# Optimization experiments

Measured on AMD Instinct MI355X. Metric: run time of the kernel, lower is better.

The kernel has to match this reference:

```python
import jax, jax.numpy as jnp
import numpy as np

NEG = -9e10


def _gat_layer(h_in, adj_mask, W, a, alpha, concat):
    # h_in: [N, Fin], W: [Fin, Fout], a: [2*Fout, 1]
    h = h_in @ W                                  # [N, Fout]
    Fout = W.shape[1]
    a1 = a[:Fout, 0]                              # [Fout]
    a2 = a[Fout:, 0]                              # [Fout]
    # e[i,j] = leakyrelu(h_i . a1 + h_j . a2)  (decomposed repeat+cat score)
    s1 = h @ a1                                   # [N]
    s2 = h @ a2                                   # [N]
    e = jax.nn.leaky_relu(s1[:, None] + s2[None, :], negative_slope=alpha)  # [N, N]
    e = jnp.where(adj_mask, e, NEG)
    att = jax.nn.softmax(e, axis=1)               # [N, N]
    h_prime = att @ h                             # [N, Fout]
    return jax.nn.elu(h_prime) if concat else h_prime


def setup_inputs() -> dict:
    key = jax.random.key(0)
    ks = jax.random.split(key, 6)
    N, nfeat, nhid, nheads, nout = 4096, 512, 64, 8, 56
    x = jax.random.normal(ks[0], (N, nfeat), dtype=jnp.float32)
    adj = jax.random.randint(ks[1], (N, N), 0, 2, dtype=jnp.int32)
    Ws = jax.random.normal(ks[2], (nheads, nfeat, nhid), dtype=jnp.float32) * 0.05
    As = jax.random.normal(ks[3], (nheads, 2 * nhid, 1), dtype=jnp.float32) * 0.05
    W_out = jax.random.normal(ks[4], (nhid, nout), dtype=jnp.float32) * 0.05
    a_out = jax.random.normal(ks[5], (2 * nout, 1), dtype=jnp.float32) * 0.05
    return {"x": x, "adj": adj, "Ws": Ws, "As": As, "W_out": W_out, "a_out": a_out}


def reference(x, adj, Ws, As, W_out, a_out):
    alpha = 0.2
    nheads = Ws.shape[0]
    adj_mask = adj > 0
    # dropout is identity in eval mode
    heads = jax.vmap(lambda W, a: _gat_layer(x, adj_mask, W, a, alpha, True))(Ws, As)
    z = jnp.sum(heads, axis=0) / nheads           # [N, nhid] (heads averaged, per source)
    out = _gat_layer(z, adj_mask, W_out, a_out, alpha, False)
    out = jax.nn.elu(out)                         # [N, 56]
    return jax.nn.softmax(out, axis=1)
```

## Files before the change

kernel.cpp:

```cpp
#include <hip/hip_runtime.h>
#include <hip/hip_bf16.h>
#include <math.h>


#define GN 4096
#define GNH 8
#define LOG2E 1.4426950408889634f

typedef __bf16 bf16x8 __attribute__((ext_vector_type(8)));
typedef float f32x4 __attribute__((ext_vector_type(4)));

#if defined(__has_builtin)
#if __has_builtin(__builtin_amdgcn_exp2f)
#define FAST_EXP2(x) __builtin_amdgcn_exp2f(x)
#endif
#if __has_builtin(__builtin_amdgcn_perm)
#define FAST_PERM(a, b, s) __builtin_amdgcn_perm((a), (b), (s))
#endif
#endif
#ifndef FAST_EXP2
#define FAST_EXP2(x) __expf((x)*0.6931471805599453f)
#endif
#ifndef FAST_PERM
__device__ inline unsigned FAST_PERM(unsigned a, unsigned b, unsigned) {
    return (a & 0xFFFF0000u) | (b >> 16);
}
#endif

__device__ inline unsigned hi_pack2(float w0, float w1) {
    unsigned u0 = __float_as_uint(w0) + 0x8000u;
    unsigned u1 = __float_as_uint(w1) + 0x8000u;
    return FAST_PERM(u1, u0, 0x07060302u);
}

__global__ __launch_bounds__(256) void prep(const int* __restrict__ adj,
                                            const float* __restrict__ x,
                                            const float* __restrict__ Ws,
                                            unsigned long long* __restrict__ adjb,
                                            unsigned short* __restrict__ xh,
                                            unsigned short* __restrict__ wth) {
    const int b = blockIdx.x;
    const int tid = threadIdx.x;
    if (b < 16384) {
        const int wv = tid >> 6, lane = tid & 63;
        const size_t ebase = ((size_t)b * 4 + wv) * 256;
        unsigned long long m[4];
        #pragma unroll
        for (int e = 0; e < 4; ++e)
            m[e] = __ballot(adj[ebase + e * 64 + lane] > 0);
        if (lane == 0) {
            #pragma unroll
            for (int e = 0; e < 4; ++e) adjb[(ebase >> 6) + e] = m[e];
        }
    } else if (b < 17408) {
        int gid = (b - 16384) * 256 + tid;
        int i = gid >> 6, c64 = gid & 63;
        const float* xp = x + (size_t)i * 512 + c64 * 8;
        float4 a = *(const float4*)xp;
        float4 v = *(const float4*)(xp + 4);
        unsigned hp[4];
        hp[0] = hi_pack2(a.x, a.y);
        hp[1] = hi_pack2(a.z, a.w);
        hp[2] = hi_pack2(v.x, v.y);
        hp[3] = hi_pack2(v.z, v.w);
        int il = i & 63, kt = c64 >> 3, c = c64 & 7;
        size_t base = ((size_t)(i >> 6) * 8 + kt) * 4096 + il * 64 + ((c ^ (il & 7)) * 8);
        *(uint4*)&xh[base] = *(uint4*)hp;
    } else {
        __shared__ float t[64][65];
        int b2 = b - 17408;
        int head = b2 >> 3, k0 = (b2 & 7) * 64;
        #pragma unroll
        for (int it = 0; it < 4; ++it) {
            int e = (tid + it * 256) * 4;
            int kl = e >> 6, f4 = e & 63;
            float4 v = *(const float4*)&Ws[((size_t)head * 512 + k0 + kl) * 64 + f4];
            t[f4 + 0][kl] = v.x; t[f4 + 1][kl] = v.y;
            t[f4 + 2][kl] = v.z; t[f4 + 3][kl] = v.w;
        }
        __syncthreads();
        int f = tid >> 2;
        #pragma unroll
        for (int p = 0; p < 2; ++p) {
            int c = (tid & 3) * 2 + p;
            unsigned hp[4];
            #pragma unroll
            for (int pp = 0; pp < 4; ++pp)
                hp[pp] = hi_pack2(t[f][c * 8 + 2 * pp], t[f][c * 8 + 2 * pp + 1]);
            size_t base = (size_t)b2 * 4096 + f * 64 + ((c ^ (f & 7)) * 8);
            *(uint4*)&wth[base] = *(uint4*)hp;
        }
    }
}

__global__ __launch_bounds__(256) void gemm_fused(const unsigned short* __restrict__ xh,
                                                  const unsigned short* __restrict__ wth,
                                                  const float* __restrict__ As,
                                                  unsigned short* __restrict__ imgh,
                                                  float* __restrict__ rL,
                                                  float2* __restrict__ ebL) {
    __shared__ __align__(16) unsigned short lds[2][2][4096];
    const int tid = threadIdx.x;
    const int head = blockIdx.x;
    const int itile = blockIdx.y;
    const int i0 = itile * 64;
    const unsigned short* srcs[2] = {xh + (size_t)itile * 8 * 4096,
                                     wth + (size_t)head * 8 * 4096};
    const int lane = tid & 63, wv_ = tid >> 6;
    const int mi = (wv_ & 1) * 32, fi = (wv_ >> 1) * 32;
    const int row = lane & 15, quad = lane >> 4;
    f32x4 acc[2][2] = {};

    #define GSTAGE(buf, kt)                                                                \
        do {                                                                               \
            _Pragma("unroll")                                                              \
            for (int q_ = 0; q_ < 2; ++q_) {                                               \
                const unsigned short* s_ = srcs[q_] + (size_t)(kt) * 4096;                 \
                _Pragma("unroll")                                                          \
                for (int c_ = 0; c_ < 2; ++c_)                                             \
                    __builtin_amdgcn_global_load_lds(                                      \
                        (const __attribute__((address_space(1))) unsigned int*)(s_ + c_ * 2048 + tid * 8), \
                        (__attribute__((address_space(3))) unsigned int*)&lds[buf][q_][c_ * 2048 + tid * 8], \
                        16, 0, 0);                                                         \
            }                                                                              \
        } while (0)

    GSTAGE(0, 0);
    for (int kt = 0; kt < 8; ++kt) {
        __syncthreads();
        const int cur = kt & 1;
        if (kt + 1 < 8) GSTAGE(cur ^ 1, kt + 1);
        #pragma unroll
        for (int ks = 0; ks < 2; ++ks) {
            bf16x8 ah[2], bh[2];
            #pragma unroll
            for (int t = 0; t < 2; ++t) {
                const int m_ = mi + t * 16 + row;
                const int offa = m_ * 64 + (((ks * 4 + quad) ^ (m_ & 7)) * 8);
                ah[t] = *(const bf16x8*)&lds[cur][0][offa];
                const int f_ = fi + t * 16 + row;
                const int offb = f_ * 64 + (((ks * 4 + quad) ^ (f_ & 7)) * 8);
                bh[t] = *(const bf16x8*)&lds[cur][1][offb];
            }
            #pragma unroll
            for (int mt = 0; mt < 2; ++mt)
                #pragma unroll
                for (int nt = 0; nt < 2; ++nt)
                    acc[mt][nt] = __builtin_amdgcn_mfma_f32_16x16x32_bf16(ah[mt], bh[nt], acc[mt][nt], 0, 0, 0);
        }
    }
    #undef GSTAGE
    __syncthreads();
    float* ht = (float*)&lds[0][0][0];
    #pragma unroll
    for (int mt = 0; mt < 2; ++mt)
        #pragma unroll
        for (int nt = 0; nt < 2; ++nt)
            #pragma unroll
            for (int r = 0; r < 4; ++r)
                ht[(mi + mt * 16 + quad * 4 + r) * 68 + fi + nt * 16 + row] = acc[mt][nt][r];
    __syncthreads();
    {
        const int rrow = tid >> 2, seg = (tid & 3) * 16;
        const float* ah = As + head * 128;
        float p1 = 0.f, p2 = 0.f;
        #pragma unroll
        for (int c = 0; c < 16; ++c) {
            float v = ht[rrow * 68 + seg + c];
            p1 += v * ah[seg + c];
            p2 += v * ah[64 + seg + c];
        }
        p1 += __shfl_xor(p1, 1); p1 += __shfl_xor(p1, 2);
        p2 += __shfl_xor(p2, 1); p2 += __shfl_xor(p2, 2);
        if ((tid & 3) == 0) {
            const int gi = i0 + rrow;
            rL[head * GN + gi] = FAST_EXP2(0.8f * p1 * LOG2E);
            float2 e;
            e.x = FAST_EXP2(p2 * LOG2E);
            e.y = FAST_EXP2(0.2f * p2 * LOG2E);
            ebL[head * GN + gi] = e;
        }
    }
    {
        const int f = tid >> 2;
        size_t base = ((size_t)head * 64 + itile) * 4096 + (size_t)f * 64;
        #pragma unroll
        for (int p = 0; p < 2; ++p) {
            int c = (tid & 3) * 2 + p;
            unsigned hp[4];
            #pragma unroll
            for (int pp = 0; pp < 4; ++pp)
                hp[pp] = hi_pack2(ht[(c * 8 + 2 * pp) * 68 + f], ht[(c * 8 + 2 * pp + 1) * 68 + f]);
            int off = (c ^ (f & 7)) * 8;
            *(uint4*)&imgh[base + off] = *(uint4*)hp;
        }
    }
}

template <int NCHUNK>
__global__ __launch_bounds__(256, 4) void attn10(const unsigned short* __restrict__ imgh,
                                                 const float* __restrict__ rg,
                                                 const float2* __restrict__ ebg,
                                                 const unsigned long long* __restrict__ adjb,
                                                 float* __restrict__ pO,
                                                 float* __restrict__ pd) {
    __shared__ __align__(16) unsigned short hb[2][8192];
    const int tid = threadIdx.x;
    const int lane = tid & 63, wv = tid >> 6;
    const int row = lane & 15, quad = lane >> 4;
    const int head = blockIdx.y / NCHUNK;
    const int chunk = blockIdx.y % NCHUNK;
    const int i0 = blockIdx.x * 64;
    const int jb = chunk * (GN / NCHUNK);
    const int njt = (GN / NCHUNK) / 64;
    const int njp = njt >> 1;
    const int jt0 = jb >> 6;
    const unsigned short* ih = imgh + (size_t)head * (64 * GN);
    const float2* ebh = ebg + (size_t)head * GN;
    const int gr = i0 + wv * 16 + row;
    const float rv = rg[head * GN + gr];
    const unsigned long long* adjr = adjb + (size_t)gr * 64 + jt0;

    f32x4 acc[4] = {};
    f32x4 accd = {};
    union { unsigned u[4]; bf16x8 v; } ones;
    #pragma unroll
    for (int q = 0; q < 4; ++q) ones.u[q] = 0x3F803F80u;

    #define STAGE2(buf, T)                                                                 \
        do {                                                                               \
            const unsigned short* gh_ = ih + (size_t)(T) * 4096;                           \
            _Pragma("unroll")                                                              \
            for (int c_ = 0; c_ < 4; ++c_)                                                 \
                __builtin_amdgcn_global_load_lds(                                          \
                    (const __attribute__((address_space(1))) unsigned int*)(gh_ + c_ * 2048 + tid * 8), \
                    (__attribute__((address_space(3))) unsigned int*)&hb[buf][c_ * 2048 + tid * 8],     \
                    16, 0, 0);                                                             \
        } while (0)

    #define CTILE(cur, half, WD, F00, F01, F02, F03, F10, F11, F12, F13)                   \
        do {                                                                               \
            _Pragma("unroll")                                                              \
            for (int ks = 0; ks < 2; ++ks) {                                               \
                const int kb = ks * 32 + quad * 8;                                         \
                const unsigned bits = (unsigned)((WD) >> kb) & 0xFFu;                      \
                const float4 e4[4] = {ks ? F10 : F00, ks ? F11 : F01,                      \
                                      ks ? F12 : F02, ks ? F13 : F03};                     \
                union { unsigned u[4]; bf16x8 v; } wfr;                                    \
                _Pragma("unroll")                                                          \
                for (int p = 0; p < 4; ++p) {                                              \
                    const float4 e = e4[p];                          \
                    const float m0 = (float)((bits >> (2 * p)) & 1u);                      \
                    const float m1 = (float)((bits >> (2 * p + 1)) & 1u);                  \
                    const float w0 = fmaxf(rv * e.x, e.y) * m0;                            \
                    const float w1 = fmaxf(rv * e.z, e.w) * m1;                            \
                    wfr.u[p] = hi_pack2(w0, w1);                                           \
                }                                                                          \
                accd = __builtin_amdgcn_mfma_f32_16x16x32_bf16(wfr.v, ones.v, accd, 0, 0, 0); \
                _Pragma("unroll")                                                          \
                for (int nt = 0; nt < 4; ++nt) {                                           \
                    const int f = nt * 16 + row;                                           \
                    const int off = (half) * 4096 + f * 64 + (((ks * 4 + quad) ^ (f & 7)) * 8); \
                    bf16x8 bh = *(const bf16x8*)&hb[cur][off];                             \
                    acc[nt] = __builtin_amdgcn_mfma_f32_16x16x32_bf16(wfr.v, bh, acc[nt], 0, 0, 0); \
                }                                                                          \
            }                                                                              \
        } while (0)

    STAGE2(0, jt0);
    const float2* ebp = ebh + jb + quad * 8;
    unsigned long long wdn = adjr[0];
    float4 n00 = *(const float4*)(ebp + 0);
    float4 n01 = *(const float4*)(ebp + 2);
    float4 n02 = *(const float4*)(ebp + 4);
    float4 n03 = *(const float4*)(ebp + 6);
    float4 n10 = *(const float4*)(ebp + 32);
    float4 n11 = *(const float4*)(ebp + 34);
    float4 n12 = *(const float4*)(ebp + 36);
    float4 n13 = *(const float4*)(ebp + 38);

    for (int ph = 0; ph < njp; ++ph) {
        __syncthreads();
        const int cur = ph & 1;
        if (ph + 1 < njp) STAGE2(cur ^ 1, jt0 + 2 * (ph + 1));
        {
            const unsigned long long wd = wdn;
            const float4 f00 = n00, f01 = n01, f02 = n02, f03 = n03;
            const float4 f10 = n10, f11 = n11, f12 = n12, f13 = n13;
            {
                const int tn = 2 * ph + 1;
                wdn = adjr[tn];
                const float2* ebn = ebp + tn * 64;
                n00 = *(const float4*)(ebn + 0);
                n01 = *(const float4*)(ebn + 2);
                n02 = *(const float4*)(ebn + 4);
                n03 = *(const float4*)(ebn + 6);
                n10 = *(const float4*)(ebn + 32);
                n11 = *(const float4*)(ebn + 34);
                n12 = *(const float4*)(ebn + 36);
                n13 = *(const float4*)(ebn + 38);
            }
            CTILE(cur, 0, wd, f00, f01, f02, f03, f10, f11, f12, f13);
        }
        {
            const unsigned long long wd = wdn;
            const float4 f00 = n00, f01 = n01, f02 = n02, f03 = n03;
            const float4 f10 = n10, f11 = n11, f12 = n12, f13 = n13;
            if (ph + 1 < njp) {
                const int tn = 2 * ph + 2;
                wdn = adjr[tn];
                const float2* ebn = ebp + tn * 64;
                n00 = *(const float4*)(ebn + 0);
                n01 = *(const float4*)(ebn + 2);
                n02 = *(const float4*)(ebn + 4);
                n03 = *(const float4*)(ebn + 6);
                n10 = *(const float4*)(ebn + 32);
                n11 = *(const float4*)(ebn + 34);
                n12 = *(const float4*)(ebn + 36);
                n13 = *(const float4*)(ebn + 38);
            }
            CTILE(cur, 1, wd, f00, f01, f02, f03, f10, f11, f12, f13);
        }
    }
    #undef STAGE2
    #undef CTILE
    float* o = pO + (size_t)blockIdx.y * (GN * 64);
    #pragma unroll
    for (int r = 0; r < 4; ++r) {
        const int grow = i0 + wv * 16 + quad * 4 + r;
        #pragma unroll
        for (int nt = 0; nt < 4; ++nt)
            o[(size_t)grow * 64 + nt * 16 + row] = acc[nt][r];
    }
    if (row == 0) {
        #pragma unroll
        for (int r = 0; r < 4; ++r)
            pd[blockIdx.y * GN + i0 + wv * 16 + quad * 4 + r] = accd[r];
    }
}

__global__ __launch_bounds__(256) void mid(const float* __restrict__ pO,
                                           const float* __restrict__ pd,
                                           const float* __restrict__ Wo,
                                           const float* __restrict__ ao,
                                           unsigned short* __restrict__ img2h,
                                           float* __restrict__ rbL,
                                           float2* __restrict__ eb2L) {
    __shared__ __align__(16) float zt[16][68];
    __shared__ float Wl[64 * 57];
    __shared__ float invd[8][16];
    const int tid = threadIdx.x;
    const int i0 = blockIdx.x * 16;
    for (int idx = tid; idx < 64 * 56; idx += 256) {
        int k = idx / 56, c = idx - k * 56;
        Wl[k * 57 + c] = Wo[idx];
    }
    if (tid < 128) {
        int hd = tid >> 4, r = tid & 15;
        invd[hd][r] = 1.f / (pd[(2 * hd) * GN + i0 + r] + pd[(2 * hd + 1) * GN + i0 + r]);
    }
    __syncthreads();
    #pragma unroll
    for (int it = 0; it < 4; ++it) {
        int e = it * 256 + tid;
        int r = e >> 6, f = e & 63;
        size_t base = (size_t)(i0 + r) * 64 + f;
        float s = 0.f;
        #pragma unroll
        for (int hd = 0; hd < GNH; ++hd) {
            float o = pO[(size_t)(2 * hd) * (GN * 64) + base] +
                      pO[(size_t)(2 * hd + 1) * (GN * 64) + base];
            float v = o * invd[hd][r];
            s += v > 0.f ? v : FAST_EXP2(v * LOG2E) - 1.f;
        }
        zt[r][f] = s * 0.125f;
    }
    __syncthreads();
    const int rrow = tid >> 4, cseg = (tid & 15) * 4;
    float hreg[4] = {0.f, 0.f, 0.f, 0.f};
    for (int k0 = 0; k0 < 64; k0 += 4) {
        float4 zv = *(const float4*)&zt[rrow][k0];
        #pragma unroll
        for (int c = 0; c < 4; ++c) {
            int col = cseg + c;
            if (col < 56)
                hreg[c] += zv.x * Wl[k0 * 57 + col] + zv.y * Wl[(k0 + 1) * 57 + col] +
                           zv.z * Wl[(k0 + 2) * 57 + col] + zv.w * Wl[(k0 + 3) * 57 + col];
        }
    }
    {
        float p1 = 0.f, p2 = 0.f;
        #pragma unroll
        for (int c = 0; c < 4; ++c) {
            int col = cseg + c;
            if (col < 56) {
                p1 += hreg[c] * ao[col];
                p2 += hreg[c] * ao[56 + col];
            }
        }
        p1 += __shfl_xor(p1, 1); p1 += __shfl_xor(p1, 2);
        p1 += __shfl_xor(p1, 4); p1 += __shfl_xor(p1, 8);
        p2 += __shfl_xor(p2, 1); p2 += __shfl_xor(p2, 2);
        p2 += __shfl_xor(p2, 4); p2 += __shfl_xor(p2, 8);
        if ((tid & 15) == 0) {
            rbL[i0 + rrow] = FAST_EXP2(0.8f * p1 * LOG2E);
            float2 e;
            e.x = FAST_EXP2(p2 * LOG2E);
            e.y = FAST_EXP2(0.2f * p2 * LOG2E);
            eb2L[i0 + rrow] = e;
        }
    }
    __syncthreads();
    #pragma unroll
    for (int c = 0; c < 4; ++c) zt[rrow][cseg + c] = (cseg + c < 56) ? hreg[c] : 0.f;
    __syncthreads();
    if (tid < 128) {
        const int jt = i0 >> 6;
        const int cbase = (i0 & 63) >> 3;
        const int f = tid >> 1, c = cbase + (tid & 1);
        const int lr = (tid & 1) * 8;
        unsigned hp[4];
        #pragma unroll
        for (int pp = 0; pp < 4; ++pp)
            hp[pp] = hi_pack2(zt[lr + 2 * pp][f], zt[lr + 2 * pp + 1][f]);
        size_t base = (size_t)jt * 4096 + f * 64 + ((c ^ (f & 7)) * 8);
        *(uint4*)&img2h[base] = *(uint4*)hp;
    }
}

__global__ __launch_bounds__(256) void fink2(const float* __restrict__ pO,
                                             const float* __restrict__ pd,
                                             float* __restrict__ out) {
    const int lane = threadIdx.x & 63;
    const int w = threadIdx.x >> 6;
    const int i = blockIdx.x * 4 + w;
    float o = 0.f, d = 0.f;
    #pragma unroll
    for (int c = 0; c < 16; ++c) d += pd[c * GN + i];
    if (lane < 56) {
        #pragma unroll
        for (int c = 0; c < 16; ++c) o += pO[(size_t)c * (GN * 64) + (size_t)i * 64 + lane];
    }
    float v = -1e30f;
    if (lane < 56) {
        float t = o / d;
        v = t > 0.f ? t : expm1f(t);
    }
    float m = v;
    #pragma unroll
    for (int off = 32; off; off >>= 1) m = fmaxf(m, __shfl_down(m, off));
    m = __shfl(m, 0);
    float p = (lane < 56) ? __expf(v - m) : 0.f;
    float s = p;
    #pragma unroll
    for (int off = 32; off; off >>= 1) s += __shfl_down(s, off);
    s = __shfl(s, 0);
    if (lane < 56) out[(size_t)i * 56 + lane] = p / s;
}

extern "C" void kernel_launch(void* const* d_in, const int* in_sizes, int n_in,
                              void* d_out, int out_size, void* d_ws, size_t ws_size,
                              hipStream_t stream) {
    const float* x    = (const float*)d_in[0];
    const int*   adj  = (const int*)d_in[1];
    const float* Ws   = (const float*)d_in[2];
    const float* As   = (const float*)d_in[3];
    const float* Wo   = (const float*)d_in[4];
    const float* ao   = (const float*)d_in[5];
    float* out = (float*)d_out;

    char* ws = (char*)d_ws;
    unsigned long long* adjb = (unsigned long long*)(ws + 0);
    unsigned short* img1h = (unsigned short*)(ws + 2097152);
    float* pO    = (float*)(ws + 6291456);
    unsigned short* x_hi = (unsigned short*)(ws + 6291456);
    float* pd    = (float*)(ws + 23068672);
    float* rL    = (float*)(ws + 23330816);
    float2* ebL  = (float2*)(ws + 23461888);
    float* rbL   = (float*)(ws + 23724032);
    float2* eb2L = (float2*)(ws + 23740416);
    unsigned short* img2h = (unsigned short*)(ws + 23773184);
    unsigned short* WT_hi = (unsigned short*)(ws + 24297472);

    prep<<<17472, 256, 0, stream>>>(adj, x, Ws, adjb, x_hi, WT_hi);
    gemm_fused<<<dim3(8, 64), 256, 0, stream>>>(x_hi, WT_hi, As, img1h, rL, ebL);
    attn10<2><<<dim3(64, 16), 256, 0, stream>>>(img1h, rL, ebL, adjb, pO, pd);
    mid<<<256, 256, 0, stream>>>(pO, pd, Wo, ao, img2h, rbL, eb2L);
    attn10<16><<<dim3(64, 16), 256, 0, stream>>>(img2h, rbL, eb2L, adjb, pO, pd);
    fink2<<<1024, 256, 0, stream>>>(pO, pd, out);
}
```

Baseline: 205.6 us.

## Switch operands to fp16 and compute attention weights with packed half math

Replaces bf16 truncation packing with fp16 packed conversion (cvt_pkrtz) and uses fp16 MFMA everywhere. The per-column exp factors are stored as packed fp16 pairs, which halves their load traffic in the attention kernel. The weight computation now uses packed half max/multiply with bit masks instead of float ops, converts and float-to-int mask multiplies. The risk is fp16 range overflow for exp values and accuracy differences.

Result: faster. 185.2 us (-9.9%).

```diff
diff --git a/kernel.cpp b/kernel.cpp
--- a/kernel.cpp
+++ b/kernel.cpp
@@ -7,7 +7,9 @@
 #define GNH 8
 #define LOG2E 1.4426950408889634f
 
-typedef __bf16 bf16x8 __attribute__((ext_vector_type(8)));
+typedef _Float16 f16x8 __attribute__((ext_vector_type(8)));
+typedef _Float16 f16x2 __attribute__((ext_vector_type(2)));
+typedef __fp16 fp16x2_raw __attribute__((ext_vector_type(2)));
 typedef float f32x4 __attribute__((ext_vector_type(4)));
 
 #if defined(__has_builtin)
@@ -15,22 +17,29 @@
 #define FAST_EXP2(x) __builtin_amdgcn_exp2f(x)
 #endif
 #if __has_builtin(__builtin_amdgcn_perm)
-#define FAST_PERM(a, b, s) __builtin_amdgcn_perm((a), (b), (s))
+#define MASK_PERM(h, l) __builtin_amdgcn_perm((h), (l), 0x05040100u)
+#endif
+#if __has_builtin(__builtin_amdgcn_cvt_pkrtz)
+#define HAVE_PKRTZ 1
 #endif
 #endif
 #ifndef FAST_EXP2
 #define FAST_EXP2(x) __expf((x)*0.6931471805599453f)
 #endif
-#ifndef FAST_PERM
-__device__ inline unsigned FAST_PERM(unsigned a, unsigned b, unsigned) {
-    return (a & 0xFFFF0000u) | (b >> 16);
-}
-#endif
-
-__device__ inline unsigned hi_pack2(float w0, float w1) {
-    unsigned u0 = __float_as_uint(w0) + 0x8000u;
-    unsigned u1 = __float_as_uint(w1) + 0x8000u;
-    return FAST_PERM(u1, u0, 0x07060302u);
+#ifndef MASK_PERM
+#define MASK_PERM(h, l) (((h) & 0xFFFF0000u) | ((l) & 0xFFFFu))
+#endif
+
+__device__ inline unsigned pk_f16(float a, float b) {
+#ifdef HAVE_PKRTZ
+    union { fp16x2_raw h; unsigned u; } r;
+    r.h = __builtin_amdgcn_cvt_pkrtz(a, b);
+    return r.u;
+#else
+    union { _Float16 h; unsigned short s; } x, y;
+    x.h = (_Float16)a; y.h = (_Float16)b;
+    return (unsigned)x.s | ((unsigned)y.s << 16);
+#endif
 }
 
 __global__ __launch_bounds__(256) void prep(const int* __restrict__ adj,
@@ -59,10 +68,10 @@
         float4 a = *(const float4*)xp;
         float4 v = *(const float4*)(xp + 4);
         unsigned hp[4];
-        hp[0] = hi_pack2(a.x, a.y);
-        hp[1] = hi_pack2(a.z, a.w);
-        hp[2] = hi_pack2(v.x, v.y);
-        hp[3] = hi_pack2(v.z, v.w);
+        hp[0] = pk_f16(a.x, a.y);
+        hp[1] = pk_f16(a.z, a.w);
+        hp[2] = pk_f16(v.x, v.y);
+        hp[3] = pk_f16(v.z, v.w);
         int il = i & 63, kt = c64 >> 3, c = c64 & 7;
         size_t base = ((size_t)(i >> 6) * 8 + kt) * 4096 + il * 64 + ((c ^ (il & 7)) * 8);
         *(uint4*)&xh[base] = *(uint4*)hp;
@@ -86,7 +95,7 @@
             unsigned hp[4];
             #pragma unroll
             for (int pp = 0; pp < 4; ++pp)
-                hp[pp] = hi_pack2(t[f][c * 8 + 2 * pp], t[f][c * 8 + 2 * pp + 1]);
+                hp[pp] = pk_f16(t[f][c * 8 + 2 * pp], t[f][c * 8 + 2 * pp + 1]);
             size_t base = (size_t)b2 * 4096 + f * 64 + ((c ^ (f & 7)) * 8);
             *(uint4*)&wth[base] = *(uint4*)hp;
         }
@@ -98,7 +107,7 @@
                                                   const float* __restrict__ As,
                                                   unsigned short* __restrict__ imgh,
                                                   float* __restrict__ rL,
-                                                  float2* __restrict__ ebL) {
+                                                  uint2* __restrict__ ebL) {
     __shared__ __align__(16) unsigned short lds[2][2][4096];
     const int tid = threadIdx.x;
     const int head = blockIdx.x;
@@ -132,21 +141,21 @@
         if (kt + 1 < 8) GSTAGE(cur ^ 1, kt + 1);
         #pragma unroll
         for (int ks = 0; ks < 2; ++ks) {
-            bf16x8 ah[2], bh[2];
+            f16x8 ah[2], bh[2];
             #pragma unroll
             for (int t = 0; t < 2; ++t) {
                 const int m_ = mi + t * 16 + row;
                 const int offa = m_ * 64 + (((ks * 4 + quad) ^ (m_ & 7)) * 8);
-                ah[t] = *(const bf16x8*)&lds[cur][0][offa];
+                ah[t] = *(const f16x8*)&lds[cur][0][offa];
                 const int f_ = fi + t * 16 + row;
                 const int offb = f_ * 64 + (((ks * 4 + quad) ^ (f_ & 7)) * 8);
-                bh[t] = *(const bf16x8*)&lds[cur][1][offb];
+                bh[t] = *(const f16x8*)&lds[cur][1][offb];
             }
             #pragma unroll
             for (int mt = 0; mt < 2; ++mt)
                 #pragma unroll
                 for (int nt = 0; nt < 2; ++nt)
-                    acc[mt][nt] = __builtin_amdgcn_mfma_f32_16x16x32_bf16(ah[mt], bh[nt], acc[mt][nt], 0, 0, 0);
+                    acc[mt][nt] = __builtin_amdgcn_mfma_f32_16x16x32_f16(ah[mt], bh[nt], acc[mt][nt], 0, 0, 0);
         }
     }
     #undef GSTAGE
@@ -172,13 +181,18 @@
         }
         p1 += __shfl_xor(p1, 1); p1 += __shfl_xor(p1, 2);
         p2 += __shfl_xor(p2, 1); p2 += __shfl_xor(p2, 2);
-        if ((tid & 3) == 0) {
-            const int gi = i0 + rrow;
-            rL[head * GN + gi] = FAST_EXP2(0.8f * p1 * LOG2E);
-            float2 e;
-            e.x = FAST_EXP2(p2 * LOG2E);
-            e.y = FAST_EXP2(0.2f * p2 * LOG2E);
-            ebL[head * GN + gi] = e;
+        const float r_ = FAST_EXP2(0.8f * p1 * LOG2E);
+        const float B_ = FAST_EXP2(p2 * LOG2E);
+        const float b_ = FAST_EXP2(0.2f * p2 * LOG2E);
+        const float Bo = __shfl_xor(B_, 4);
+        const float bo = __shfl_xor(b_, 4);
+        const int gi = i0 + rrow;
+        if ((tid & 3) == 0) rL[head * GN + gi] = r_;
+        if ((tid & 7) == 0) {
+            uint2 e;
+            e.x = pk_f16(B_, Bo);
+            e.y = pk_f16(b_, bo);
+            ebL[head * (GN / 2) + (gi >> 1)] = e;
         }
     }
     {
@@ -190,7 +204,7 @@
             unsigned hp[4];
             #pragma unroll
             for (int pp = 0; pp < 4; ++pp)
-                hp[pp] = hi_pack2(ht[(c * 8 + 2 * pp) * 68 + f], ht[(c * 8 + 2 * pp + 1) * 68 + f]);
+                hp[pp] = pk_f16(ht[(c * 8 + 2 * pp) * 68 + f], ht[(c * 8 + 2 * pp + 1) * 68 + f]);
             int off = (c ^ (f & 7)) * 8;
             *(uint4*)&imgh[base + off] = *(uint4*)hp;
         }
@@ -198,9 +212,9 @@
 }
 
 template <int NCHUNK>
-__global__ __launch_bounds__(256, 4) void attn10(const unsigned short* __restrict__ imgh,
+__global__ __launch_bounds__(256, 4) void attn12(const unsigned short* __restrict__ imgh,
                                                  const float* __restrict__ rg,
-                                                 const float2* __restrict__ ebg,
+                                                 const uint2* __restrict__ ebg,
                                                  const unsigned long long* __restrict__ adjb,
                                                  float* __restrict__ pO,
                                                  float* __restrict__ pd) {
@@ -216,16 +230,19 @@
     const int njp = njt >> 1;
     const int jt0 = jb >> 6;
     const unsigned short* ih = imgh + (size_t)head * (64 * GN);
-    const float2* ebh = ebg + (size_t)head * GN;
     const int gr = i0 + wv * 16 + row;
     const float rv = rg[head * GN + gr];
     const unsigned long long* adjr = adjb + (size_t)gr * 64 + jt0;
+    const uint4* ebq4 = (const uint4*)(ebg + (size_t)head * (GN / 2)) + (jb >> 2) + quad * 2;
+
+    const _Float16 rh = (_Float16)rv;
+    const f16x2 rv2 = {rh, rh};
 
     f32x4 acc[4] = {};
     f32x4 accd = {};
-    union { unsigned u[4]; bf16x8 v; } ones;
-    #pragma unroll
-    for (int q = 0; q < 4; ++q) ones.u[q] = 0x3F803F80u;
+    union { unsigned u[4]; f16x8 v; } ones;
+    #pragma unroll
+    for (int q = 0; q < 4; ++q) ones.u[q] = 0x3C003C00u;
 
     #define STAGE2(buf, T)                                                                 \
         do {                                                                               \
@@ -238,46 +255,40 @@
                     16, 0, 0);                                                             \
         } while (0)
 
-    #define CTILE(cur, half, WD, F00, F01, F02, F03, F10, F11, F12, F13)                   \
+    #define CTILE(cur, half, WD, A0, A1, B0, B1)                                           \
         do {                                                                               \
             _Pragma("unroll")                                                              \
             for (int ks = 0; ks < 2; ++ks) {                                               \
-                const int kb = ks * 32 + quad * 8;                                         \
-                const unsigned bits = (unsigned)((WD) >> kb) & 0xFFu;                      \
-                const float4 e4[4] = {ks ? F10 : F00, ks ? F11 : F01,                      \
-                                      ks ? F12 : F02, ks ? F13 : F03};                     \
-                union { unsigned u[4]; bf16x8 v; } wfr;                                    \
+                const unsigned bits = (unsigned)((WD) >> (ks * 32 + quad * 8)) & 0xFFu;    \
+                const uint4 ua = ks ? (B0) : (A0);                                         \
+                const uint4 ub = ks ? (B1) : (A1);                                         \
+                const unsigned Bw[4] = {ua.x, ua.z, ub.x, ub.z};                           \
+                const unsigned bw[4] = {ua.y, ua.w, ub.y, ub.w};                           \
+                union { unsigned u[4]; f16x8 v; } wfr;                                     \
                 _Pragma("unroll")                                                          \
                 for (int p = 0; p < 4; ++p) {                                              \
-                    const float4 e = e4[p];                          \
-                    const float m0 = (float)((bits >> (2 * p)) & 1u);                      \
-                    const float m1 = (float)((bits >> (2 * p + 1)) & 1u);                  \
-                    const float w0 = fmaxf(rv * e.x, e.y) * m0;                            \
-                    const float w1 = fmaxf(rv * e.z, e.w) * m1;                            \
-                    wfr.u[p] = hi_pack2(w0, w1);                                           \
+                    const unsigned lo = (unsigned)(((int)(bits << (31 - 2 * p))) >> 31);   \
+                    const unsigned hi = (unsigned)(((int)(bits << (30 - 2 * p))) >> 31);   \
+                    const unsigned msk = MASK_PERM(hi, lo);                                \
+                    union { unsigned u; f16x2 h; } B2, b2, w;                              \
+                    B2.u = Bw[p]; b2.u = bw[p];                                            \
+                    w.h = __builtin_elementwise_max(rv2 * B2.h, b2.h);                     \
+                    wfr.u[p] = w.u & msk;                                                  \
                 }                                                                          \
-                accd = __builtin_amdgcn_mfma_f32_16x16x32_bf16(wfr.v, ones.v, accd, 0, 0, 0); \
+                accd = __builtin_amdgcn_mfma_f32_16x16x32_f16(wfr.v, ones.v, accd, 0, 0, 0); \
                 _Pragma("unroll")                                                          \
                 for (int nt = 0; nt < 4; ++nt) {                                           \
                     const int f = nt * 16 + row;                                           \
                     const int off = (half) * 4096 + f * 64 + (((ks * 4 + quad) ^ (f & 7)) * 8); \
-                    bf16x8 bh = *(const bf16x8*)&hb[cur][off];                             \
-                    acc[nt] = __builtin_amdgcn_mfma_f32_16x16x32_bf16(wfr.v, bh, acc[nt], 0, 0, 0); \
+                    f16x8 bh = *(const f16x8*)&hb[cur][off];                               \
+                    acc[nt] = __builtin_amdgcn_mfma_f32_16x16x32_f16(wfr.v, bh, acc[nt], 0, 0, 0); \
                 }                                                                          \
             }                                                                              \
         } while (0)
 
     STAGE2(0, jt0);
-    const float2* ebp = ebh + jb + quad * 8;
     unsigned long long wdn = adjr[0];
-    float4 n00 = *(const float4*)(ebp + 0);
-    float4 n01 = *(const float4*)(ebp + 2);
-    float4 n02 = *(const float4*)(ebp + 4);
-    float4 n03 = *(const float4*)(ebp + 6);
-    float4 n10 = *(const float4*)(ebp + 32);
-    float4 n11 = *(const float4*)(ebp + 34);
-    float4 n12 = *(const float4*)(ebp + 36);
-    float4 n13 = *(const float4*)(ebp + 38);
+    uint4 nA0 = ebq4[0], nA1 = ebq4[1], nB0 = ebq4[8], nB1 = ebq4[9];
 
     for (int ph = 0; ph < njp; ++ph) {
         __syncthreads();
@@ -285,45 +296,30 @@
         if (ph + 1 < njp) STAGE2(cur ^ 1, jt0 + 2 * (ph + 1));
         {
             const unsigned long long wd = wdn;
-            const float4 f00 = n00, f01 = n01, f02 = n02, f03 = n03;
-            const float4 f10 = n10, f11 = n11, f12 = n12, f13 = n13;
+            const uint4 a0 = nA0, a1 = nA1, b0 = nB0, b1 = nB1;
             {
                 const int tn = 2 * ph + 1;
                 wdn = adjr[tn];
-                const float2* ebn = ebp + tn * 64;
-                n00 = *(const float4*)(ebn + 0);
-                n01 = *(const float4*)(ebn + 2);
-                n02 = *(const float4*)(ebn + 4);
-                n03 = *(const float4*)(ebn + 6);
-                n10 = *(const float4*)(ebn + 32);
-                n11 = *(const float4*)(ebn + 34);
-                n12 = *(const float4*)(ebn + 36);
-                n13 = *(const float4*)(ebn + 38);
+                nA0 = ebq4[tn * 16];     nA1 = ebq4[tn * 16 + 1];
+                nB0 = ebq4[tn * 16 + 8]; nB1 = ebq4[tn * 16 + 9];
             }
-            CTILE(cur, 0, wd, f00, f01, f02, f03, f10, f11, f12, f13);
+            CTILE(cur, 0, wd, a0, a1, b0, b1);
         }
         {
             const unsigned long long wd = wdn;
-            const float4 f00 = n00, f01 = n01, f02 = n02, f03 = n03;
-            const float4 f10 = n10, f11 = n11, f12 = n12, f13 = n13;
+            const uint4 a0 = nA0, a1 = nA1, b0 = nB0, b1 = nB1;
             if (ph + 1 < njp) {
                 const int tn = 2 * ph + 2;
                 wdn = adjr[tn];
-                const float2* ebn = ebp + tn * 64;
-                n00 = *(const float4*)(ebn + 0);
-                n01 = *(const float4*)(ebn + 2);
-                n02 = *(const float4*)(ebn + 4);
-                n03 = *(const float4*)(ebn + 6);
-                n10 = *(const float4*)(ebn + 32);
-                n11 = *(const float4*)(ebn + 34);
-                n12 = *(const float4*)(ebn + 36);
-                n13 = *(const float4*)(ebn + 38);
+                nA0 = ebq4[tn * 16];     nA1 = ebq4[tn * 16 + 1];
+                nB0 = ebq4[tn * 16 + 8]; nB1 = ebq4[tn * 16 + 9];
             }
-            CTILE(cur, 1, wd, f00, f01, f02, f03, f10, f11, f12, f13);
+            CTILE(cur, 1, wd, a0, a1, b0, b1);
         }
     }
     #undef STAGE2
     #undef CTILE
+
     float* o = pO + (size_t)blockIdx.y * (GN * 64);
     #pragma unroll
     for (int r = 0; r < 4; ++r) {
@@ -345,7 +341,7 @@
                                            const float* __restrict__ ao,
                                            unsigned short* __restrict__ img2h,
                                            float* __restrict__ rbL,
-                                           float2* __restrict__ eb2L) {
+                                           uint2* __restrict__ eb2L) {
     __shared__ __align__(16) float zt[16][68];
     __shared__ float Wl[64 * 57];
     __shared__ float invd[8][16];
@@ -402,12 +398,17 @@
         p1 += __shfl_xor(p1, 4); p1 += __shfl_xor(p1, 8);
         p2 += __shfl_xor(p2, 1); p2 += __shfl_xor(p2, 2);
         p2 += __shfl_xor(p2, 4); p2 += __shfl_xor(p2, 8);
-        if ((tid & 15) == 0) {
-            rbL[i0 + rrow] = FAST_EXP2(0.8f * p1 * LOG2E);
-            float2 e;
-            e.x = FAST_EXP2(p2 * LOG2E);
-            e.y = FAST_EXP2(0.2f * p2 * LOG2E);
-            eb2L[i0 + rrow] = e;
+        const float r_ = FAST_EXP2(0.8f * p1 * LOG2E);
+        const float B_ = FAST_EXP2(p2 * LOG2E);
+        const float b_ = FAST_EXP2(0.2f * p2 * LOG2E);
+        const float Bo = __shfl_xor(B_, 16);
+        const float bo = __shfl_xor(b_, 16);
+        if ((tid & 15) == 0) rbL[i0 + rrow] = r_;
+        if ((tid & 31) == 0) {
+            uint2 e;
+            e.x = pk_f16(B_, Bo);
+            e.y = pk_f16(b_, bo);
+            eb2L[(i0 + rrow) >> 1] = e;
         }
     }
     __syncthreads();
@@ -422,7 +423,7 @@
         unsigned hp[4];
         #pragma unroll
         for (int pp = 0; pp < 4; ++pp)
-            hp[pp] = hi_pack2(zt[lr + 2 * pp][f], zt[lr + 2 * pp + 1][f]);
+            hp[pp] = pk_f16(zt[lr + 2 * pp][f], zt[lr + 2 * pp + 1][f]);
         size_t base = (size_t)jt * 4096 + f * 64 + ((c ^ (f & 7)) * 8);
         *(uint4*)&img2h[base] = *(uint4*)hp;
     }
@@ -476,16 +477,16 @@
     unsigned short* x_hi = (unsigned short*)(ws + 6291456);
     float* pd    = (float*)(ws + 23068672);
     float* rL    = (float*)(ws + 23330816);
-    float2* ebL  = (float2*)(ws + 23461888);
+    uint2* ebL   = (uint2*)(ws + 23461888);
     float* rbL   = (float*)(ws + 23724032);
-    float2* eb2L = (float2*)(ws + 23740416);
+    uint2* eb2L  = (uint2*)(ws + 23740416);
     unsigned short* img2h = (unsigned short*)(ws + 23773184);
     unsigned short* WT_hi = (unsigned short*)(ws + 24297472);
 
     prep<<<17472, 256, 0, stream>>>(adj, x, Ws, adjb, x_hi, WT_hi);
     gemm_fused<<<dim3(8, 64), 256, 0, stream>>>(x_hi, WT_hi, As, img1h, rL, ebL);
-    attn10<2><<<dim3(64, 16), 256, 0, stream>>>(img1h, rL, ebL, adjb, pO, pd);
+    attn12<2><<<dim3(64, 16), 256, 0, stream>>>(img1h, rL, ebL, adjb, pO, pd);
     mid<<<256, 256, 0, stream>>>(pO, pd, Wo, ao, img2h, rbL, eb2L);
-    attn10<16><<<dim3(64, 16), 256, 0, stream>>>(img2h, rbL, eb2L, adjb, pO, pd);
+    attn12<16><<<dim3(64, 16), 256, 0, stream>>>(img2h, rbL, eb2L, adjb, pO, pd);
     fink2<<<1024, 256, 0, stream>>>(pO, pd, out);
 }
```
